# Performance work log

Hardware: AMD Instinct MI355X
Metric: run time of the kernel (lower is better)

Reference implementation:

```python
import jax, jax.numpy as jnp
import numpy as np

S, B, G, P = 8, 8192, 512, 16
E, H, BOT = 64, 64, 1024

def setup_inputs() -> dict:
    key = jax.random.key(0)
    k = jax.random.split(key, 9)
    in_xy = jax.random.normal(k[0], (S, B, 2), dtype=jnp.float32)
    in_dxdy = jax.random.normal(k[1], (S, B, 2), dtype=jnp.float32)
    h_states = jax.random.normal(k[2], (1, B, H), dtype=jnp.float32)
    starts = jnp.arange(G, dtype=jnp.int64) * P
    seq_start_end = jnp.stack([starts, starts + P], axis=1)
    W_emb = jax.random.normal(k[3], (2, E), dtype=jnp.float32) / jnp.sqrt(2.0)
    b_emb = jnp.zeros((E,), dtype=jnp.float32)
    W1 = jax.random.normal(k[4], (E + H, H), dtype=jnp.float32) / jnp.sqrt(float(E + H))
    b1 = jnp.zeros((H,), dtype=jnp.float32)
    W2 = jax.random.normal(k[5], (H, BOT), dtype=jnp.float32) / jnp.sqrt(float(H))
    b2 = jnp.zeros((BOT,), dtype=jnp.float32)
    return {"in_xy": in_xy, "in_dxdy": in_dxdy, "h_states": h_states,
            "seq_start_end": seq_start_end, "W_emb": W_emb, "b_emb": b_emb,
            "W1": W1, "b1": b1, "W2": W2, "b2": b2}

def reference(in_xy, in_dxdy, h_states, seq_start_end, W_emb, b_emb, W1, b1, W2, b2):
    # Uniform group size: P = batch / num_groups (groups are contiguous).
    batch = in_xy.shape[1]
    g = seq_start_end.shape[0]
    p = batch // g
    end_pos = in_xy[-1].reshape(g, p, 2)            # (G,P,2)
    h = h_states.reshape(batch, -1).reshape(g, p, -1)  # (G,P,H)
    # torch semantics: row (i*P+j) of the pair matrix uses pos[j]-pos[i], hidden[j]
    rel = end_pos[:, None, :, :] - end_pos[:, :, None, :]  # (G,P_i,P_j,2)
    emb = rel @ W_emb + b_emb                              # (G,P,P,E)
    hj = jnp.broadcast_to(h[:, None, :, :], (g, p, p, h.shape[-1]))
    x = jnp.concatenate([emb, hj], axis=-1)                # (G,P,P,E+H)
    x = jax.nn.relu(x @ W1 + b1)
    x = jax.nn.relu(x @ W2 + b2)                           # (G,P,P,BOT)
    pool = jnp.max(x, axis=2)                              # max over j -> (G,P,BOT)
    return pool.reshape(batch, -1)
```

## Files before the change

kernel.cpp:

```cpp
#include <hip/hip_runtime.h>
#include <hip/hip_bf16.h>

typedef __attribute__((ext_vector_type(8))) short bf16x8;
typedef __attribute__((ext_vector_type(4))) float f32x4;

#define NB 8192
#define NS 8

__device__ __forceinline__ unsigned short f2bf(float f) {
  union { float f; unsigned int u; } v; v.f = f;
  unsigned int r = v.u + 0x7FFFu + ((v.u >> 16) & 1u);
  return (unsigned short)(r >> 16);
}

__global__ __launch_bounds__(256) void prep_kernel(
    const float* __restrict__ W2, const float* __restrict__ W_emb,
    const float* __restrict__ b_emb, const float* __restrict__ W1,
    unsigned short* __restrict__ w2f, float* __restrict__ wc) {
  int tid = blockIdx.x * 256 + threadIdx.x;
  if (tid < 8192) {
    int lane = tid & 63;
    int ks = (tid >> 6) & 1;
    int nt = tid >> 7;
    int col = nt * 16 + (lane & 15);
    int k0 = ks * 32 + (lane >> 4) * 8;
    bf16x8 pk;
#pragma unroll
    for (int e = 0; e < 8; ++e)
      pk[e] = (short)f2bf(W2[(k0 + e) * 1024 + col]);
    *(bf16x8*)(w2f + tid * 8) = pk;
  } else if (tid < 8192 + 192) {
    int t2 = tid - 8192;
    int c = t2 >> 6, k = t2 & 63;
    float s = 0.f;
    for (int e = 0; e < 64; ++e) {
      float src = (c < 2) ? W_emb[c * 64 + e] : b_emb[e];
      s += src * W1[e * 64 + k];
    }
    wc[t2] = s;
  }
}

__global__ __launch_bounds__(512, 4) void pool_kernel(
    const float* __restrict__ in_xy, const float* __restrict__ h_states,
    const float* __restrict__ W1, const float* __restrict__ b1,
    const float* __restrict__ b2, const unsigned short* __restrict__ w2f,
    const float* __restrict__ wc, float* __restrict__ out) {
  __shared__ bf16x8 Afrag[2048];
  __shared__ float hW[16 * 68];
  __shared__ float exy[32];
  const int g = blockIdx.x;
  const int t = threadIdx.x;
  const int lane = t & 63;
  const int wv = t >> 6;

  if (t < 32) {
    int p = t & 15;
    exy[t] = in_xy[((NS - 1) * NB + g * 16 + p) * 2 + (t >> 4)];
  }

  {
    int k = t & 63;
    int j0 = t >> 6;
    const float* hbase = h_states + g * 16 * 64;
    float a0 = 0.f, a1 = 0.f;
    for (int e = 0; e < 64; ++e) {
      float w = W1[(64 + e) * 64 + k];
      a0 += hbase[j0 * 64 + e] * w;
      a1 += hbase[(j0 + 8) * 64 + e] * w;
    }
    float bb = b1[k] + wc[128 + k];
    hW[j0 * 68 + k] = a0 + bb;
    hW[(j0 + 8) * 68 + k] = a1 + bb;
  }

  float b2v[8];
#pragma unroll
  for (int u = 0; u < 8; ++u) b2v[u] = b2[wv * 128 + u * 16 + (lane & 15)];
  __syncthreads();

  {
    int i = t & 15;
    int kc = (t >> 4) & 3;
    int ks = (t >> 6) & 1;
    int k0 = ks * 32 + kc * 8;
    int jb = t >> 7;
    float w0[8], w1[8];
#pragma unroll
    for (int e = 0; e < 8; ++e) {
      w0[e] = wc[k0 + e];
      w1[e] = wc[64 + k0 + e];
    }
    float exi = exy[i], eyi = exy[16 + i];
#pragma unroll
    for (int c = 0; c < 4; ++c) {
      int j = jb + 4 * c;
      float rx = exy[j] - exi;
      float ry = exy[16 + j] - eyi;
      const f32x4* hp = (const f32x4*)&hW[j * 68 + k0];
      f32x4 h0 = hp[0], h1 = hp[1];
      float hv[8] = {h0[0], h0[1], h0[2], h0[3], h1[0], h1[1], h1[2], h1[3]};
      bf16x8 pk;
#pragma unroll
      for (int e = 0; e < 8; ++e) {
        float v = fmaf(rx, w0[e], fmaf(ry, w1[e], hv[e]));
        v = fmaxf(v, 0.f);
        pk[e] = (short)f2bf(v);
      }
      Afrag[t + 512 * c] = pk;
    }
  }
  __syncthreads();

  const int col = lane & 15;
  const int rowoff = (g * 16 + (lane >> 4) * 4) * 1024 + wv * 128 + col;
  const bf16x8* ap = Afrag + lane;
#pragma unroll
  for (int pass = 0; pass < 2; ++pass) {
    bf16x8 bfr[4][2];
#pragma unroll
    for (int u = 0; u < 4; ++u) {
      int nt = wv * 8 + pass * 4 + u;
      bfr[u][0] = *(const bf16x8*)(w2f + ((nt * 2 + 0) * 64 + lane) * 8);
      bfr[u][1] = *(const bf16x8*)(w2f + ((nt * 2 + 1) * 64 + lane) * 8);
    }
    f32x4 pool[4];
#pragma unroll
    for (int u = 0; u < 4; ++u) pool[u] = (f32x4){-3.4e38f, -3.4e38f, -3.4e38f, -3.4e38f};

    bf16x8 a0 = ap[0];
    bf16x8 a1 = ap[64];
    for (int j = 0; j < 16; ++j) {
      f32x4 acc[4];
      __builtin_amdgcn_s_setprio(1);
#pragma unroll
      for (int u = 0; u < 4; ++u) {
        f32x4 z = {0.f, 0.f, 0.f, 0.f};
        acc[u] = __builtin_amdgcn_mfma_f32_16x16x32_bf16(a0, bfr[u][0], z, 0, 0, 0);
      }
#pragma unroll
      for (int u = 0; u < 4; ++u)
        acc[u] = __builtin_amdgcn_mfma_f32_16x16x32_bf16(a1, bfr[u][1], acc[u], 0, 0, 0);
      __builtin_amdgcn_s_setprio(0);
      int jn = (j + 1) & 15;
      a0 = ap[jn * 128];
      a1 = ap[jn * 128 + 64];
#pragma unroll
      for (int u = 0; u < 4; ++u) {
#pragma unroll
        for (int r = 0; r < 4; ++r) pool[u][r] = fmaxf(pool[u][r], acc[u][r]);
      }
    }
#pragma unroll
    for (int u = 0; u < 4; ++u) {
      float bb = b2v[pass * 4 + u];
      int cbase = rowoff + (pass * 4 + u) * 16;
#pragma unroll
      for (int r = 0; r < 4; ++r)
        out[cbase + r * 1024] = fmaxf(pool[u][r] + bb, 0.f);
    }
  }
}

extern "C" void kernel_launch(void* const* d_in, const int* in_sizes, int n_in,
                              void* d_out, int out_size, void* d_ws, size_t ws_size,
                              hipStream_t stream) {
  const float* in_xy = (const float*)d_in[0];
  const float* h_states = (const float*)d_in[2];
  const float* W_emb = (const float*)d_in[4];
  const float* b_emb = (const float*)d_in[5];
  const float* W1 = (const float*)d_in[6];
  const float* b1 = (const float*)d_in[7];
  const float* W2 = (const float*)d_in[8];
  const float* b2 = (const float*)d_in[9];
  float* out = (float*)d_out;

  unsigned short* w2f = (unsigned short*)d_ws;
  float* wc = (float*)((char*)d_ws + 131072);

  prep_kernel<<<33, 256, 0, stream>>>(W2, W_emb, b_emb, W1, w2f, wc);
  pool_kernel<<<512, 512, 0, stream>>>(in_xy, h_states, W1, b1, b2, w2f, wc, out);
}
```

Before: 31.18 us.

## Precompute hidden projection with MFMA kernel and split pool blocks by output half

Moves the per-group h_states @ W1 projection out of the pool kernel into a separate MFMA-based kernel, using bf16 weights prepared in the prep kernel. It also splits each group across two 256-thread blocks that each cover half of the output columns, and loads A fragments inside an unrolled loop instead of prefetching them. This removes the scalar 64-step FMA loop from every pool block and doubles block-level parallelism. In exchange it adds a kernel launch, a global round-trip for hW, duplicated A-fragment construction in both halves, and lower precision for the hidden projection.

```diff
diff --git a/kernel.cpp b/kernel.cpp
--- a/kernel.cpp
+++ b/kernel.cpp
@@ -16,7 +16,8 @@
 __global__ __launch_bounds__(256) void prep_kernel(
     const float* __restrict__ W2, const float* __restrict__ W_emb,
     const float* __restrict__ b_emb, const float* __restrict__ W1,
-    unsigned short* __restrict__ w2f, float* __restrict__ wc) {
+    unsigned short* __restrict__ w2f, float* __restrict__ wc,
+    unsigned short* __restrict__ w1bf) {
   int tid = blockIdx.x * 256 + threadIdx.x;
   if (tid < 8192) {
     int lane = tid & 63;
@@ -38,18 +39,59 @@
       s += src * W1[e * 64 + k];
     }
     wc[t2] = s;
-  }
-}
-
-__global__ __launch_bounds__(512, 4) void pool_kernel(
-    const float* __restrict__ in_xy, const float* __restrict__ h_states,
-    const float* __restrict__ W1, const float* __restrict__ b1,
-    const float* __restrict__ b2, const unsigned short* __restrict__ w2f,
-    const float* __restrict__ wc, float* __restrict__ out) {
+  } else if (tid < 8192 + 192 + 512) {
+    int q = tid - 8384;
+    int lane = q & 63;
+    int fr = q >> 6;
+    int nt = fr >> 1, ks = fr & 1;
+    int col = nt * 16 + (lane & 15);
+    int e0 = ks * 32 + (lane >> 4) * 8;
+    bf16x8 pk;
+#pragma unroll
+    for (int e = 0; e < 8; ++e)
+      pk[e] = (short)f2bf(W1[(64 + e0 + e) * 64 + col]);
+    *(bf16x8*)(w1bf + q * 8) = pk;
+  }
+}
+
+__global__ __launch_bounds__(64) void hw_kernel(
+    const float* __restrict__ h_states, const float* __restrict__ b1,
+    const float* __restrict__ wc, const unsigned short* __restrict__ w1bf,
+    float* __restrict__ hW) {
+  const int lane = threadIdx.x;
+  const int b = blockIdx.x;
+  const int row = b * 16 + (lane & 15);
+  const int k0 = (lane >> 4) * 8;
+  const float* hp = h_states + row * 64 + k0;
+  bf16x8 a0, a1;
+#pragma unroll
+  for (int e = 0; e < 8; ++e) {
+    a0[e] = (short)f2bf(hp[e]);
+    a1[e] = (short)f2bf(hp[e + 32]);
+  }
+#pragma unroll
+  for (int nt = 0; nt < 4; ++nt) {
+    bf16x8 bf0 = *(const bf16x8*)(w1bf + ((nt * 2 + 0) * 64 + lane) * 8);
+    bf16x8 bf1 = *(const bf16x8*)(w1bf + ((nt * 2 + 1) * 64 + lane) * 8);
+    f32x4 z = {0.f, 0.f, 0.f, 0.f};
+    f32x4 acc = __builtin_amdgcn_mfma_f32_16x16x32_bf16(a0, bf0, z, 0, 0, 0);
+    acc = __builtin_amdgcn_mfma_f32_16x16x32_bf16(a1, bf1, acc, 0, 0, 0);
+    int col = nt * 16 + (lane & 15);
+    float bb = b1[col] + wc[128 + col];
+#pragma unroll
+    for (int r = 0; r < 4; ++r)
+      hW[(b * 16 + (lane >> 4) * 4 + r) * 64 + col] = acc[r] + bb;
+  }
+}
+
+__global__ __launch_bounds__(256, 4) void pool_kernel(
+    const float* __restrict__ in_xy, const float* __restrict__ b2,
+    const unsigned short* __restrict__ w2f, const float* __restrict__ wc,
+    const float* __restrict__ hW, float* __restrict__ out) {
   __shared__ bf16x8 Afrag[2048];
-  __shared__ float hW[16 * 68];
   __shared__ float exy[32];
-  const int g = blockIdx.x;
+  const int g = blockIdx.x >> 1;
+  const int half = blockIdx.x & 1;
   const int t = threadIdx.x;
   const int lane = t & 63;
   const int wv = t >> 6;
@@ -59,45 +101,31 @@
     exy[t] = in_xy[((NS - 1) * NB + g * 16 + p) * 2 + (t >> 4)];
   }
 
+  float b2v[8];
+#pragma unroll
+  for (int u = 0; u < 8; ++u)
+    b2v[u] = b2[half * 512 + wv * 128 + u * 16 + (lane & 15)];
+
+  const int i = t & 15;
+  const int kc = (t >> 4) & 3;
+  const int ks = (t >> 6) & 1;
+  const int k0 = ks * 32 + kc * 8;
+  float w0[8], w1[8];
+#pragma unroll
+  for (int e = 0; e < 8; ++e) {
+    w0[e] = wc[k0 + e];
+    w1[e] = wc[64 + k0 + e];
+  }
+  __syncthreads();
+
   {
-    int k = t & 63;
-    int j0 = t >> 6;
-    const float* hbase = h_states + g * 16 * 64;
-    float a0 = 0.f, a1 = 0.f;
-    for (int e = 0; e < 64; ++e) {
-      float w = W1[(64 + e) * 64 + k];
-      a0 += hbase[j0 * 64 + e] * w;
-      a1 += hbase[(j0 + 8) * 64 + e] * w;
-    }
-    float bb = b1[k] + wc[128 + k];
-    hW[j0 * 68 + k] = a0 + bb;
-    hW[(j0 + 8) * 68 + k] = a1 + bb;
-  }
-
-  float b2v[8];
-#pragma unroll
-  for (int u = 0; u < 8; ++u) b2v[u] = b2[wv * 128 + u * 16 + (lane & 15)];
-  __syncthreads();
-
-  {
-    int i = t & 15;
-    int kc = (t >> 4) & 3;
-    int ks = (t >> 6) & 1;
-    int k0 = ks * 32 + kc * 8;
-    int jb = t >> 7;
-    float w0[8], w1[8];
-#pragma unroll
-    for (int e = 0; e < 8; ++e) {
-      w0[e] = wc[k0 + e];
-      w1[e] = wc[64 + k0 + e];
-    }
     float exi = exy[i], eyi = exy[16 + i];
 #pragma unroll
-    for (int c = 0; c < 4; ++c) {
-      int j = jb + 4 * c;
+    for (int c = 0; c < 8; ++c) {
+      int j = (t >> 7) + 2 * c;
       float rx = exy[j] - exi;
       float ry = exy[16 + j] - eyi;
-      const f32x4* hp = (const f32x4*)&hW[j * 68 + k0];
+      const f32x4* hp = (const f32x4*)(hW + (g * 16 + j) * 64 + k0);
       f32x4 h0 = hp[0], h1 = hp[1];
       float hv[8] = {h0[0], h0[1], h0[2], h0[3], h1[0], h1[1], h1[2], h1[3]};
       bf16x8 pk;
@@ -107,20 +135,19 @@
         v = fmaxf(v, 0.f);
         pk[e] = (short)f2bf(v);
       }
-      Afrag[t + 512 * c] = pk;
+      Afrag[t + 256 * c] = pk;
     }
   }
   __syncthreads();
 
-  const int col = lane & 15;
-  const int rowoff = (g * 16 + (lane >> 4) * 4) * 1024 + wv * 128 + col;
+  const int rowbase = (g * 16 + (lane >> 4) * 4) * 1024 + half * 512 + wv * 128 + (lane & 15);
   const bf16x8* ap = Afrag + lane;
 #pragma unroll
   for (int pass = 0; pass < 2; ++pass) {
     bf16x8 bfr[4][2];
 #pragma unroll
     for (int u = 0; u < 4; ++u) {
-      int nt = wv * 8 + pass * 4 + u;
+      int nt = half * 32 + wv * 8 + pass * 4 + u;
       bfr[u][0] = *(const bf16x8*)(w2f + ((nt * 2 + 0) * 64 + lane) * 8);
       bfr[u][1] = *(const bf16x8*)(w2f + ((nt * 2 + 1) * 64 + lane) * 8);
     }
@@ -128,9 +155,10 @@
 #pragma unroll
     for (int u = 0; u < 4; ++u) pool[u] = (f32x4){-3.4e38f, -3.4e38f, -3.4e38f, -3.4e38f};
 
-    bf16x8 a0 = ap[0];
-    bf16x8 a1 = ap[64];
+#pragma unroll 4
     for (int j = 0; j < 16; ++j) {
+      bf16x8 a0 = ap[j * 128];
+      bf16x8 a1 = ap[j * 128 + 64];
       f32x4 acc[4];
       __builtin_amdgcn_s_setprio(1);
 #pragma unroll
@@ -142,9 +170,6 @@
       for (int u = 0; u < 4; ++u)
         acc[u] = __builtin_amdgcn_mfma_f32_16x16x32_bf16(a1, bfr[u][1], acc[u], 0, 0, 0);
       __builtin_amdgcn_s_setprio(0);
-      int jn = (j + 1) & 15;
-      a0 = ap[jn * 128];
-      a1 = ap[jn * 128 + 64];
 #pragma unroll
       for (int u = 0; u < 4; ++u) {
 #pragma unroll
@@ -154,10 +179,9 @@
 #pragma unroll
     for (int u = 0; u < 4; ++u) {
       float bb = b2v[pass * 4 + u];
-      int cbase = rowoff + (pass * 4 + u) * 16;
 #pragma unroll
       for (int r = 0; r < 4; ++r)
-        out[cbase + r * 1024] = fmaxf(pool[u][r] + bb, 0.f);
+        out[rowbase + r * 1024 + (pass * 4 + u) * 16] = fmaxf(pool[u][r] + bb, 0.f);
     }
   }
 }
@@ -177,7 +201,10 @@
 
   unsigned short* w2f = (unsigned short*)d_ws;
   float* wc = (float*)((char*)d_ws + 131072);
-
-  prep_kernel<<<33, 256, 0, stream>>>(W2, W_emb, b_emb, W1, w2f, wc);
-  pool_kernel<<<512, 512, 0, stream>>>(in_xy, h_states, W1, b1, b2, w2f, wc, out);
-}
+  unsigned short* w1bf = (unsigned short*)((char*)d_ws + 132096);
+  float* hW = (float*)((char*)d_ws + 262144);
+
+  prep_kernel<<<35, 256, 0, stream>>>(W2, W_emb, b_emb, W1, w2f, wc, w1bf);
+  hw_kernel<<<512, 64, 0, stream>>>(h_states, b1, wc, w1bf, hW);
+  pool_kernel<<<1024, 256, 0, stream>>>(in_xy, b2, w2f, wc, hW, out);
+}
```

After: 29.82 us. -4.4%, faster.
